# Kernel optimization log

Measured on AMD Instinct MI355X. Metric: run time of the kernel, lower is better.

Reference implementation:

```python
import jax, jax.numpy as jnp
import numpy as np

BATCH = 2048
OUT_DIM = 50257                      # output_dim = input feature dim
LEVELS = 2
LEVEL_SIZE = int(np.ceil(OUT_DIM ** (1.0 / LEVELS)))  # 225


def setup_inputs() -> dict:
    key = jax.random.key(0)
    k_x, k_w0, k_w1 = jax.random.split(key, 3)
    # glorot-ish scale for weights so softmax logits are well behaved
    w_scale = (2.0 / (OUT_DIM + LEVEL_SIZE)) ** 0.5
    return {
        "x": jax.random.normal(k_x, (BATCH, OUT_DIM), dtype=jnp.float32),
        "W0": jax.random.normal(k_w0, (OUT_DIM, LEVEL_SIZE), dtype=jnp.float32) * w_scale,
        "W1": jax.random.normal(k_w1, (OUT_DIM, LEVEL_SIZE), dtype=jnp.float32) * w_scale,
        "b0": jnp.zeros((LEVEL_SIZE,), dtype=jnp.float32),
        "b1": jnp.zeros((LEVEL_SIZE,), dtype=jnp.float32),
    }


def reference(x, W0, W1, b0, b1):
    # per-level softmax heads: [B, L]
    h0 = jax.nn.softmax(x @ W0 + b0, axis=-1)
    h1 = jax.nn.softmax(x @ W1 + b1, axis=-1)
    # outer product per sample, flattened: [B, L*L] (replaces nested theano.scan)
    path = (h0[:, :, None] * h1[:, None, :]).reshape(x.shape[0], -1)
    # truncate to output_dim, as in original output[:, :self.output_dim]
    return path[:, :OUT_DIM]
```

## Files before the change

### kernel.cpp

```cpp
#include <hip/hip_runtime.h>
#include <stdint.h>
#include <math.h>


#define BATCH   2048
#define KDIM    50257
#define LSZ     225
#define HOFF    240
#define NPAD    480
#define BK      32
#define BM      128
#define NT      1571
#define TILE_B  30720
#define A_BYTES 16384
#define BUF_B   47104
#define LDS_TOT 94208
#define WSCALE  1024.0f

typedef __attribute__((ext_vector_type(8))) _Float16 f16x8;
typedef __attribute__((ext_vector_type(4))) float    f32x4;

__device__ __forceinline__ unsigned short f2h(float f) {
  return __builtin_bit_cast(unsigned short, (_Float16)f);
}
__device__ __forceinline__ int swzr(int r) { return ((r >> 1) & 3) << 4; }

__global__ __launch_bounds__(512) void hs_prep(const float* __restrict__ W0,
                                               const float* __restrict__ W1,
                                               unsigned char* __restrict__ wt) {
  const int kt = blockIdx.x;
  const int k0 = kt * BK;
  unsigned char* tb = wt + (size_t)kt * TILE_B;
  for (int idx = threadIdx.x; idx < NPAD * 8; idx += 512) {
    const int n = idx >> 3, c4 = idx & 7;
    const float* src = nullptr;
    if (n < HOFF) { if (n < LSZ) src = W0 + n; }
    else          { if (n - HOFF < LSZ) src = W1 + (n - HOFF); }
    unsigned short he[4];
#pragma unroll
    for (int e = 0; e < 4; ++e) {
      const int k = k0 + c4 * 4 + e;
      float v = (src != nullptr && k < KDIM) ? src[(size_t)k * LSZ] * WSCALE : 0.0f;
      he[e] = f2h(v);
    }
    const int jp = (c4 * 8) ^ swzr(n);
    *(ushort4*)(tb + n * 64 + jp) = make_ushort4(he[0], he[1], he[2], he[3]);
  }
}

__global__ __launch_bounds__(512, 2) void hs_gemm(
    const float* __restrict__ x, const unsigned char* __restrict__ wt,
    float* __restrict__ partials, int ksplit, int tpc) {
  extern __shared__ __align__(16) unsigned char smem[];
  const int bid   = blockIdx.x;
  const int chunk = bid % ksplit;
  const int mtile = bid / ksplit;
  const int t0 = chunk * tpc;
  int t1 = t0 + tpc; if (t1 > NT) t1 = NT;
  const int m0 = mtile * BM;
  const int tid = threadIdx.x;
  const int lane = tid & 63, wid = tid >> 6;
  const int wm = wid >> 1, wn = wid & 1;
  const int jl  = (lane >> 4) * 16;
  const int l15 = lane & 15;

  const int arow0 = tid >> 3, c4 = tid & 7;
  const int arow1 = arow0 + 64;
  const float* xr0 = x + (size_t)(m0 + arow0) * KDIM + c4 * 4;
  const float* xr1 = xr0 + (size_t)64 * KDIM;
  const int aoff0 = arow0 * 64 + ((c4 * 8) ^ swzr(arow0));
  const int aoff1 = arow1 * 64 + ((c4 * 8) ^ swzr(arow1));

  f32x4 acc[2][15];
#pragma unroll
  for (int mf = 0; mf < 2; ++mf)
#pragma unroll
    for (int nf = 0; nf < 15; ++nf)
      acc[mf][nf] = f32x4{0.f, 0.f, 0.f, 0.f};

  auto stageB = [&](int kt, int buf) {
    const unsigned char* src = wt + (size_t)kt * TILE_B + lane * 16;
    unsigned char* dstb = smem + buf * BUF_B;
#pragma unroll
    for (int c = 0; c < 4; ++c) {
      const int cc = wid + c * 8;
      if (cc < 30) {
        __builtin_amdgcn_global_load_lds(
            (const __attribute__((address_space(1))) unsigned int*)(src + cc * 1024),
            (__attribute__((address_space(3))) unsigned int*)(dstb + cc * 1024),
            16, 0, 0);
      }
    }
  };

  auto loadA = [&](int kt, f32x4& v0, f32x4& v1) {
    const int kb = kt * BK + c4 * 4;
    const float* p0 = xr0 + (size_t)kt * BK;
    const float* p1 = xr1 + (size_t)kt * BK;
    if (kb + 4 <= KDIM) {
      __builtin_memcpy(&v0, p0, 16);
      __builtin_memcpy(&v1, p1, 16);
    } else {
#pragma unroll
      for (int e = 0; e < 4; ++e) {
        v0[e] = (kb + e < KDIM) ? p0[e] : 0.f;
        v1[e] = (kb + e < KDIM) ? p1[e] : 0.f;
      }
    }
  };

  auto writeA = [&](int buf, const f32x4& v0, const f32x4& v1) {
    unsigned char* ab = smem + buf * BUF_B + TILE_B;
    unsigned short h0e[4], l0e[4], h1e[4], l1e[4];
#pragma unroll
    for (int e = 0; e < 4; ++e) {
      const _Float16 h = (_Float16)v0[e];
      h0e[e] = __builtin_bit_cast(unsigned short, h);
      l0e[e] = f2h(v0[e] - (float)h);
      const _Float16 g = (_Float16)v1[e];
      h1e[e] = __builtin_bit_cast(unsigned short, g);
      l1e[e] = f2h(v1[e] - (float)g);
    }
    *(ushort4*)(ab + aoff0)        = make_ushort4(h0e[0], h0e[1], h0e[2], h0e[3]);
    *(ushort4*)(ab + 8192 + aoff0) = make_ushort4(l0e[0], l0e[1], l0e[2], l0e[3]);
    *(ushort4*)(ab + aoff1)        = make_ushort4(h1e[0], h1e[1], h1e[2], h1e[3]);
    *(ushort4*)(ab + 8192 + aoff1) = make_ushort4(l1e[0], l1e[1], l1e[2], l1e[3]);
  };

  auto compute = [&](int buf) {
    const unsigned char* bb = smem + buf * BUF_B;
    const unsigned char* ab = bb + TILE_B;
    f16x8 ah[2], al[2];
#pragma unroll
    for (int mf = 0; mf < 2; ++mf) {
      const int m = wm * 32 + mf * 16 + l15;
      const int off = m * 64 + (jl ^ swzr(m));
      ah[mf] = *(const f16x8*)(ab + off);
      al[mf] = *(const f16x8*)(ab + 8192 + off);
    }
#pragma unroll
    for (int nf = 0; nf < 15; ++nf) {
      const int n = wn * 240 + nf * 16 + l15;
      const int off = n * 64 + (jl ^ swzr(n));
      const f16x8 bw = *(const f16x8*)(bb + off);
#pragma unroll
      for (int mf = 0; mf < 2; ++mf) {
        acc[mf][nf] = __builtin_amdgcn_mfma_f32_16x16x32_f16(ah[mf], bw, acc[mf][nf], 0, 0, 0);
        acc[mf][nf] = __builtin_amdgcn_mfma_f32_16x16x32_f16(al[mf], bw, acc[mf][nf], 0, 0, 0);
      }
    }
  };

  if (t0 < t1) {
    f32x4 v0, v1;
    stageB(t0, 0);
    loadA(t0, v0, v1);
    writeA(0, v0, v1);
    __syncthreads();
    int buf = 0;
    for (int t = t0; t < t1; ++t) {
      const bool more = (t + 1 < t1);
      if (more) {
        stageB(t + 1, buf ^ 1);
        loadA(t + 1, v0, v1);
      }
      compute(buf);
      if (more) writeA(buf ^ 1, v0, v1);
      __syncthreads();
      buf ^= 1;
    }
  }

  float* pout = partials + ((size_t)chunk * BATCH + m0) * NPAD;
#pragma unroll
  for (int mf = 0; mf < 2; ++mf)
#pragma unroll
    for (int nf = 0; nf < 15; ++nf)
#pragma unroll
      for (int r = 0; r < 4; ++r) {
        const int row = wm * 32 + mf * 16 + (lane >> 4) * 4 + r;
        const int col = wn * 240 + nf * 16 + l15;
        pout[(size_t)row * NPAD + col] = acc[mf][nf][r];
      }
}

__global__ __launch_bounds__(512) void hs_finish(
    const float* __restrict__ partials, const float* __restrict__ b0,
    const float* __restrict__ b1, float* __restrict__ out, int ksplit) {
  const int b = blockIdx.x;
  __shared__ float lg[NPAD];
  __shared__ float red[4];
  const int tid = threadIdx.x;
  if (tid < NPAD) {
    float v = 0.f;
    for (int c = 0; c < ksplit; ++c)
      v += partials[((size_t)c * BATCH + b) * NPAD + tid];
    v *= (1.0f / WSCALE);
    if (tid < LSZ) v += b0[tid];
    else if (tid >= HOFF && tid < HOFF + LSZ) v += b1[tid - HOFF];
    lg[tid] = v;
  }
  __syncthreads();
  const int wid = tid >> 6, lane = tid & 63;
  if (wid < 2) {
    const int base = wid * HOFF;
    float m = -1e30f;
    for (int i = lane; i < LSZ; i += 64) m = fmaxf(m, lg[base + i]);
#pragma unroll
    for (int s = 32; s; s >>= 1) m = fmaxf(m, __shfl_xor(m, s));
    float sum = 0.f;
    for (int i = lane; i < LSZ; i += 64) sum += __expf(lg[base + i] - m);
#pragma unroll
    for (int s = 32; s; s >>= 1) sum += __shfl_xor(sum, s);
    if (lane == 0) { red[wid * 2] = m; red[wid * 2 + 1] = 1.0f / sum; }
  }
  __syncthreads();
  if (tid < NPAD) {
    const int h = (tid >= HOFF) ? 1 : 0;
    const int off = tid - (h ? HOFF : 0);
    float hv = 0.f;
    if (off < LSZ) hv = __expf(lg[tid] - red[2 * h]) * red[2 * h + 1];
    lg[tid] = hv;
  }
  __syncthreads();
  const size_t ob = (size_t)b * KDIM;
  for (int f = tid; f < KDIM; f += 512) {
    const int i = f / LSZ;
    const int j = f - i * LSZ;
    out[ob + f] = lg[i] * lg[HOFF + j];
  }
}

extern "C" void kernel_launch(void* const* d_in, const int* in_sizes, int n_in,
                              void* d_out, int out_size, void* d_ws, size_t ws_size,
                              hipStream_t stream) {
  (void)in_sizes; (void)n_in; (void)out_size;
  const float* x  = (const float*)d_in[0];
  const float* W0 = (const float*)d_in[1];
  const float* W1 = (const float*)d_in[2];
  const float* b0 = (const float*)d_in[3];
  const float* b1 = (const float*)d_in[4];
  float* out = (float*)d_out;
  unsigned char* ws = (unsigned char*)d_ws;

  const size_t WT_BYTES  = (size_t)NT * TILE_B;
  const size_t PER_CHUNK = (size_t)BATCH * NPAD * sizeof(float);
  int ksplit = 16;
  if (ws_size > WT_BYTES) {
    const int kmax = (int)((ws_size - WT_BYTES) / PER_CHUNK);
    if (ksplit > kmax) ksplit = kmax;
  } else {
    ksplit = 1;
  }
  if (ksplit < 1) ksplit = 1;
  float* partials = (float*)(ws + WT_BYTES);
  const int tpc = (NT + ksplit - 1) / ksplit;

  hs_prep<<<dim3(NT), dim3(512), 0, stream>>>(W0, W1, ws);
  hipFuncSetAttribute((const void*)hs_gemm,
                      hipFuncAttributeMaxDynamicSharedMemorySize, LDS_TOT);
  hs_gemm<<<dim3(16 * ksplit), dim3(512), LDS_TOT, stream>>>(x, ws, partials, ksplit, tpc);
  hs_finish<<<dim3(BATCH), dim3(512), 0, stream>>>(partials, b0, b1, out, ksplit);
}
```

Before: 349.9 us.

## Load A fragments directly from global into MFMA registers, skip LDS staging

```diff
diff --git a/kernel.cpp b/kernel.cpp
--- a/kernel.cpp
+++ b/kernel.cpp
@@ -12,9 +12,8 @@
 #define BM      128
 #define NT      1571
 #define TILE_B  30720
-#define A_BYTES 16384
-#define BUF_B   47104
-#define LDS_TOT 94208
+#define BUF_B   30720
+#define LDS_TOT 61440
 #define WSCALE  1024.0f
 
 typedef __attribute__((ext_vector_type(8))) _Float16 f16x8;
@@ -24,6 +23,8 @@
   return __builtin_bit_cast(unsigned short, (_Float16)f);
 }
 __device__ __forceinline__ int swzr(int r) { return ((r >> 1) & 3) << 4; }
+
+#define ASM_VMCNT0() asm volatile("s_waitcnt vmcnt(0)" ::: "memory")
 
 __global__ __launch_bounds__(512) void hs_prep(const float* __restrict__ W0,
                                                const float* __restrict__ W1,
@@ -62,14 +63,11 @@
   const int lane = tid & 63, wid = tid >> 6;
   const int wm = wid >> 1, wn = wid & 1;
   const int jl  = (lane >> 4) * 16;
+  const int ko  = (lane >> 4) * 8;
   const int l15 = lane & 15;
 
-  const int arow0 = tid >> 3, c4 = tid & 7;
-  const int arow1 = arow0 + 64;
-  const float* xr0 = x + (size_t)(m0 + arow0) * KDIM + c4 * 4;
-  const float* xr1 = xr0 + (size_t)64 * KDIM;
-  const int aoff0 = arow0 * 64 + ((c4 * 8) ^ swzr(arow0));
-  const int aoff1 = arow1 * 64 + ((c4 * 8) ^ swzr(arow1));
+  const float* ar0 = x + (size_t)(m0 + wm * 32 + l15) * KDIM + ko;
+  const float* ar1 = ar0 + (size_t)16 * KDIM;
 
   f32x4 acc[2][15];
 #pragma unroll
@@ -77,6 +75,9 @@
 #pragma unroll
     for (int nf = 0; nf < 15; ++nf)
       acc[mf][nf] = f32x4{0.f, 0.f, 0.f, 0.f};
+
+  f32x4 g00, g01, g10, g11;
+  f16x8 ah0, al0, ah1, al1;
 
   auto stageB = [&](int kt, int buf) {
     const unsigned char* src = wt + (size_t)kt * TILE_B + lane * 16;
@@ -93,79 +94,70 @@
     }
   };
 
-  auto loadA = [&](int kt, f32x4& v0, f32x4& v1) {
-    const int kb = kt * BK + c4 * 4;
-    const float* p0 = xr0 + (size_t)kt * BK;
-    const float* p1 = xr1 + (size_t)kt * BK;
-    if (kb + 4 <= KDIM) {
-      __builtin_memcpy(&v0, p0, 16);
-      __builtin_memcpy(&v1, p1, 16);
+  auto gloadA = [&](int kt) {
+    const int kb = kt * BK + ko;
+    const float* p0 = ar0 + (size_t)kt * BK;
+    const float* p1 = ar1 + (size_t)kt * BK;
+    if (kb + 8 <= KDIM) {
+      __builtin_memcpy(&g00, p0, 16);  __builtin_memcpy(&g01, p0 + 4, 16);
+      __builtin_memcpy(&g10, p1, 16);  __builtin_memcpy(&g11, p1 + 4, 16);
     } else {
 #pragma unroll
       for (int e = 0; e < 4; ++e) {
-        v0[e] = (kb + e < KDIM) ? p0[e] : 0.f;
-        v1[e] = (kb + e < KDIM) ? p1[e] : 0.f;
-      }
-    }
-  };
-
-  auto writeA = [&](int buf, const f32x4& v0, const f32x4& v1) {
-    unsigned char* ab = smem + buf * BUF_B + TILE_B;
-    unsigned short h0e[4], l0e[4], h1e[4], l1e[4];
+        g00[e] = (kb + e < KDIM)     ? p0[e]     : 0.f;
+        g01[e] = (kb + 4 + e < KDIM) ? p0[4 + e] : 0.f;
+        g10[e] = (kb + e < KDIM)     ? p1[e]     : 0.f;
+        g11[e] = (kb + 4 + e < KDIM) ? p1[4 + e] : 0.f;
+      }
+    }
+  };
+
+  auto convertA = [&]() {
 #pragma unroll
     for (int e = 0; e < 4; ++e) {
-      const _Float16 h = (_Float16)v0[e];
-      h0e[e] = __builtin_bit_cast(unsigned short, h);
-      l0e[e] = f2h(v0[e] - (float)h);
-      const _Float16 g = (_Float16)v1[e];
-      h1e[e] = __builtin_bit_cast(unsigned short, g);
-      l1e[e] = f2h(v1[e] - (float)g);
-    }
-    *(ushort4*)(ab + aoff0)        = make_ushort4(h0e[0], h0e[1], h0e[2], h0e[3]);
-    *(ushort4*)(ab + 8192 + aoff0) = make_ushort4(l0e[0], l0e[1], l0e[2], l0e[3]);
-    *(ushort4*)(ab + aoff1)        = make_ushort4(h1e[0], h1e[1], h1e[2], h1e[3]);
-    *(ushort4*)(ab + 8192 + aoff1) = make_ushort4(l1e[0], l1e[1], l1e[2], l1e[3]);
+      const _Float16 h0 = (_Float16)g00[e];
+      ah0[e] = h0;          al0[e] = (_Float16)(g00[e] - (float)h0);
+      const _Float16 h1 = (_Float16)g01[e];
+      ah0[4 + e] = h1;      al0[4 + e] = (_Float16)(g01[e] - (float)h1);
+      const _Float16 h2 = (_Float16)g10[e];
+      ah1[e] = h2;          al1[e] = (_Float16)(g10[e] - (float)h2);
+      const _Float16 h3 = (_Float16)g11[e];
+      ah1[4 + e] = h3;      al1[4 + e] = (_Float16)(g11[e] - (float)h3);
+    }
   };
 
   auto compute = [&](int buf) {
     const unsigned char* bb = smem + buf * BUF_B;
-    const unsigned char* ab = bb + TILE_B;
-    f16x8 ah[2], al[2];
-#pragma unroll
-    for (int mf = 0; mf < 2; ++mf) {
-      const int m = wm * 32 + mf * 16 + l15;
-      const int off = m * 64 + (jl ^ swzr(m));
-      ah[mf] = *(const f16x8*)(ab + off);
-      al[mf] = *(const f16x8*)(ab + 8192 + off);
-    }
 #pragma unroll
     for (int nf = 0; nf < 15; ++nf) {
       const int n = wn * 240 + nf * 16 + l15;
       const int off = n * 64 + (jl ^ swzr(n));
       const f16x8 bw = *(const f16x8*)(bb + off);
-#pragma unroll
-      for (int mf = 0; mf < 2; ++mf) {
-        acc[mf][nf] = __builtin_amdgcn_mfma_f32_16x16x32_f16(ah[mf], bw, acc[mf][nf], 0, 0, 0);
-        acc[mf][nf] = __builtin_amdgcn_mfma_f32_16x16x32_f16(al[mf], bw, acc[mf][nf], 0, 0, 0);
-      }
+      acc[0][nf] = __builtin_amdgcn_mfma_f32_16x16x32_f16(ah0, bw, acc[0][nf], 0, 0, 0);
+      acc[0][nf] = __builtin_amdgcn_mfma_f32_16x16x32_f16(al0, bw, acc[0][nf], 0, 0, 0);
+      acc[1][nf] = __builtin_amdgcn_mfma_f32_16x16x32_f16(ah1, bw, acc[1][nf], 0, 0, 0);
+      acc[1][nf] = __builtin_amdgcn_mfma_f32_16x16x32_f16(al1, bw, acc[1][nf], 0, 0, 0);
     }
   };
 
   if (t0 < t1) {
-    f32x4 v0, v1;
     stageB(t0, 0);
-    loadA(t0, v0, v1);
-    writeA(0, v0, v1);
+    gloadA(t0);
+    ASM_VMCNT0();
+    convertA();
     __syncthreads();
     int buf = 0;
     for (int t = t0; t < t1; ++t) {
       const bool more = (t + 1 < t1);
       if (more) {
         stageB(t + 1, buf ^ 1);
-        loadA(t + 1, v0, v1);
+        gloadA(t + 1);
       }
       compute(buf);
-      if (more) writeA(buf ^ 1, v0, v1);
+      if (more) {
+        ASM_VMCNT0();
+        convertA();
+      }
       __syncthreads();
       buf ^= 1;
     }
```

New measurement: 373.8 us. 1.07x slower.

## Use 12 waves per GEMM block with a 4x3 warp grid to cut accumulators

Applied to the files above, without the earlier changes.

```diff
diff --git a/kernel.cpp b/kernel.cpp
--- a/kernel.cpp
+++ b/kernel.cpp
@@ -48,7 +48,7 @@
   }
 }
 
-__global__ __launch_bounds__(512, 2) void hs_gemm(
+__global__ __launch_bounds__(768, 3) void hs_gemm(
     const float* __restrict__ x, const unsigned char* __restrict__ wt,
     float* __restrict__ partials, int ksplit, int tpc) {
   extern __shared__ __align__(16) unsigned char smem[];
@@ -60,30 +60,28 @@
   const int m0 = mtile * BM;
   const int tid = threadIdx.x;
   const int lane = tid & 63, wid = tid >> 6;
-  const int wm = wid >> 1, wn = wid & 1;
+  const int wm = wid & 3, wn = wid >> 2;
   const int jl  = (lane >> 4) * 16;
   const int l15 = lane & 15;
 
-  const int arow0 = tid >> 3, c4 = tid & 7;
-  const int arow1 = arow0 + 64;
-  const float* xr0 = x + (size_t)(m0 + arow0) * KDIM + c4 * 4;
-  const float* xr1 = xr0 + (size_t)64 * KDIM;
-  const int aoff0 = arow0 * 64 + ((c4 * 8) ^ swzr(arow0));
-  const int aoff1 = arow1 * 64 + ((c4 * 8) ^ swzr(arow1));
-
-  f32x4 acc[2][15];
+  const int arow = tid >> 2, c8 = tid & 3;
+  const bool astg = (tid < 512);
+  const float* xr = x + (size_t)(m0 + arow) * KDIM + c8 * 8;
+  const int aoff = arow * 64 + ((c8 * 16) ^ swzr(arow));
+
+  f32x4 acc[2][10];
 #pragma unroll
   for (int mf = 0; mf < 2; ++mf)
 #pragma unroll
-    for (int nf = 0; nf < 15; ++nf)
+    for (int nf = 0; nf < 10; ++nf)
       acc[mf][nf] = f32x4{0.f, 0.f, 0.f, 0.f};
 
   auto stageB = [&](int kt, int buf) {
     const unsigned char* src = wt + (size_t)kt * TILE_B + lane * 16;
     unsigned char* dstb = smem + buf * BUF_B;
 #pragma unroll
-    for (int c = 0; c < 4; ++c) {
-      const int cc = wid + c * 8;
+    for (int c = 0; c < 3; ++c) {
+      const int cc = wid + c * 12;
       if (cc < 30) {
         __builtin_amdgcn_global_load_lds(
             (const __attribute__((address_space(1))) unsigned int*)(src + cc * 1024),
@@ -94,37 +92,38 @@
   };
 
   auto loadA = [&](int kt, f32x4& v0, f32x4& v1) {
-    const int kb = kt * BK + c4 * 4;
-    const float* p0 = xr0 + (size_t)kt * BK;
-    const float* p1 = xr1 + (size_t)kt * BK;
-    if (kb + 4 <= KDIM) {
-      __builtin_memcpy(&v0, p0, 16);
-      __builtin_memcpy(&v1, p1, 16);
+    if (!astg) return;
+    const int kb = kt * BK + c8 * 8;
+    const float* p = xr + (size_t)kt * BK;
+    if (kb + 8 <= KDIM) {
+      __builtin_memcpy(&v0, p, 16);
+      __builtin_memcpy(&v1, p + 4, 16);
     } else {
 #pragma unroll
       for (int e = 0; e < 4; ++e) {
-        v0[e] = (kb + e < KDIM) ? p0[e] : 0.f;
-        v1[e] = (kb + e < KDIM) ? p1[e] : 0.f;
+        v0[e] = (kb + e < KDIM)     ? p[e]     : 0.f;
+        v1[e] = (kb + 4 + e < KDIM) ? p[4 + e] : 0.f;
       }
     }
   };
 
   auto writeA = [&](int buf, const f32x4& v0, const f32x4& v1) {
+    if (!astg) return;
     unsigned char* ab = smem + buf * BUF_B + TILE_B;
-    unsigned short h0e[4], l0e[4], h1e[4], l1e[4];
+    unsigned short he[8], le[8];
 #pragma unroll
     for (int e = 0; e < 4; ++e) {
       const _Float16 h = (_Float16)v0[e];
-      h0e[e] = __builtin_bit_cast(unsigned short, h);
-      l0e[e] = f2h(v0[e] - (float)h);
+      he[e] = __builtin_bit_cast(unsigned short, h);
+      le[e] = f2h(v0[e] - (float)h);
       const _Float16 g = (_Float16)v1[e];
-      h1e[e] = __builtin_bit_cast(unsigned short, g);
-      l1e[e] = f2h(v1[e] - (float)g);
-    }
-    *(ushort4*)(ab + aoff0)        = make_ushort4(h0e[0], h0e[1], h0e[2], h0e[3]);
-    *(ushort4*)(ab + 8192 + aoff0) = make_ushort4(l0e[0], l0e[1], l0e[2], l0e[3]);
-    *(ushort4*)(ab + aoff1)        = make_ushort4(h1e[0], h1e[1], h1e[2], h1e[3]);
-    *(ushort4*)(ab + 8192 + aoff1) = make_ushort4(l1e[0], l1e[1], l1e[2], l1e[3]);
+      he[4 + e] = __builtin_bit_cast(unsigned short, g);
+      le[4 + e] = f2h(v1[e] - (float)g);
+    }
+    *(ushort4*)(ab + aoff)            = make_ushort4(he[0], he[1], he[2], he[3]);
+    *(ushort4*)(ab + aoff + 8)        = make_ushort4(he[4], he[5], he[6], he[7]);
+    *(ushort4*)(ab + 8192 + aoff)     = make_ushort4(le[0], le[1], le[2], le[3]);
+    *(ushort4*)(ab + 8192 + aoff + 8) = make_ushort4(le[4], le[5], le[6], le[7]);
   };
 
   auto compute = [&](int buf) {
@@ -139,8 +138,8 @@
       al[mf] = *(const f16x8*)(ab + 8192 + off);
     }
 #pragma unroll
-    for (int nf = 0; nf < 15; ++nf) {
-      const int n = wn * 240 + nf * 16 + l15;
+    for (int nf = 0; nf < 10; ++nf) {
+      const int n = wn * 160 + nf * 16 + l15;
       const int off = n * 64 + (jl ^ swzr(n));
       const f16x8 bw = *(const f16x8*)(bb + off);
 #pragma unroll
@@ -175,11 +174,11 @@
 #pragma unroll
   for (int mf = 0; mf < 2; ++mf)
 #pragma unroll
-    for (int nf = 0; nf < 15; ++nf)
+    for (int nf = 0; nf < 10; ++nf)
 #pragma unroll
       for (int r = 0; r < 4; ++r) {
         const int row = wm * 32 + mf * 16 + (lane >> 4) * 4 + r;
-        const int col = wn * 240 + nf * 16 + l15;
+        const int col = wn * 160 + nf * 16 + l15;
         pout[(size_t)row * NPAD + col] = acc[mf][nf][r];
       }
 }
@@ -259,6 +258,6 @@
   hs_prep<<<dim3(NT), dim3(512), 0, stream>>>(W0, W1, ws);
   hipFuncSetAttribute((const void*)hs_gemm,
                       hipFuncAttributeMaxDynamicSharedMemorySize, LDS_TOT);
-  hs_gemm<<<dim3(16 * ksplit), dim3(512), LDS_TOT, stream>>>(x, ws, partials, ksplit, tpc);
+  hs_gemm<<<dim3(16 * ksplit), dim3(768), LDS_TOT, stream>>>(x, ws, partials, ksplit, tpc);
   hs_finish<<<dim3(BATCH), dim3(512), 0, stream>>>(partials, b0, b1, out, ksplit);
 }
```

Result: no change. 346.3 us (-1.0%).

## Drop x hi/lo fp16 split and double the K tile to 64

Applied to the files above, without the earlier changes.

```diff
diff --git a/kernel.cpp b/kernel.cpp
--- a/kernel.cpp
+++ b/kernel.cpp
@@ -8,13 +8,13 @@
 #define LSZ     225
 #define HOFF    240
 #define NPAD    480
-#define BK      32
+#define BK      64
 #define BM      128
-#define NT      1571
-#define TILE_B  30720
+#define NT      786
+#define TILE_B  61440
 #define A_BYTES 16384
-#define BUF_B   47104
-#define LDS_TOT 94208
+#define BUF_B   77824
+#define LDS_TOT 155648
 #define WSCALE  1024.0f
 
 typedef __attribute__((ext_vector_type(8))) _Float16 f16x8;
@@ -23,7 +23,7 @@
 __device__ __forceinline__ unsigned short f2h(float f) {
   return __builtin_bit_cast(unsigned short, (_Float16)f);
 }
-__device__ __forceinline__ int swzr(int r) { return ((r >> 1) & 3) << 4; }
+__device__ __forceinline__ int swz8(int r) { return (r & 7) << 4; }
 
 __global__ __launch_bounds__(512) void hs_prep(const float* __restrict__ W0,
                                                const float* __restrict__ W1,
@@ -31,8 +31,8 @@
   const int kt = blockIdx.x;
   const int k0 = kt * BK;
   unsigned char* tb = wt + (size_t)kt * TILE_B;
-  for (int idx = threadIdx.x; idx < NPAD * 8; idx += 512) {
-    const int n = idx >> 3, c4 = idx & 7;
+  for (int idx = threadIdx.x; idx < NPAD * 16; idx += 512) {
+    const int n = idx >> 4, c4 = idx & 15;
     const float* src = nullptr;
     if (n < HOFF) { if (n < LSZ) src = W0 + n; }
     else          { if (n - HOFF < LSZ) src = W1 + (n - HOFF); }
@@ -43,8 +43,8 @@
       float v = (src != nullptr && k < KDIM) ? src[(size_t)k * LSZ] * WSCALE : 0.0f;
       he[e] = f2h(v);
     }
-    const int jp = (c4 * 8) ^ swzr(n);
-    *(ushort4*)(tb + n * 64 + jp) = make_ushort4(he[0], he[1], he[2], he[3]);
+    const int jp = (c4 * 8) ^ swz8(n);
+    *(ushort4*)(tb + n * 128 + jp) = make_ushort4(he[0], he[1], he[2], he[3]);
   }
 }
 
@@ -64,12 +64,8 @@
   const int jl  = (lane >> 4) * 16;
   const int l15 = lane & 15;
 
-  const int arow0 = tid >> 3, c4 = tid & 7;
-  const int arow1 = arow0 + 64;
-  const float* xr0 = x + (size_t)(m0 + arow0) * KDIM + c4 * 4;
-  const float* xr1 = xr0 + (size_t)64 * KDIM;
-  const int aoff0 = arow0 * 64 + ((c4 * 8) ^ swzr(arow0));
-  const int aoff1 = arow1 * 64 + ((c4 * 8) ^ swzr(arow1));
+  const int arow = tid >> 2, c16 = tid & 3;
+  const float* xr = x + (size_t)(m0 + arow) * KDIM + c16 * 16;
 
   f32x4 acc[2][15];
 #pragma unroll
@@ -82,9 +78,9 @@
     const unsigned char* src = wt + (size_t)kt * TILE_B + lane * 16;
     unsigned char* dstb = smem + buf * BUF_B;
 #pragma unroll
-    for (int c = 0; c < 4; ++c) {
+    for (int c = 0; c < 8; ++c) {
       const int cc = wid + c * 8;
-      if (cc < 30) {
+      if (cc < 60) {
         __builtin_amdgcn_global_load_lds(
             (const __attribute__((address_space(1))) unsigned int*)(src + cc * 1024),
             (__attribute__((address_space(3))) unsigned int*)(dstb + cc * 1024),
@@ -93,79 +89,76 @@
     }
   };
 
-  auto loadA = [&](int kt, f32x4& v0, f32x4& v1) {
-    const int kb = kt * BK + c4 * 4;
-    const float* p0 = xr0 + (size_t)kt * BK;
-    const float* p1 = xr1 + (size_t)kt * BK;
-    if (kb + 4 <= KDIM) {
-      __builtin_memcpy(&v0, p0, 16);
-      __builtin_memcpy(&v1, p1, 16);
+  auto loadA = [&](int kt, f32x4& v0, f32x4& v1, f32x4& v2, f32x4& v3) {
+    const int kb = kt * BK + c16 * 16;
+    const float* p = xr + (size_t)kt * BK;
+    if (kb + 16 <= KDIM) {
+      __builtin_memcpy(&v0, p, 16);      __builtin_memcpy(&v1, p + 4, 16);
+      __builtin_memcpy(&v2, p + 8, 16);  __builtin_memcpy(&v3, p + 12, 16);
     } else {
 #pragma unroll
       for (int e = 0; e < 4; ++e) {
-        v0[e] = (kb + e < KDIM) ? p0[e] : 0.f;
-        v1[e] = (kb + e < KDIM) ? p1[e] : 0.f;
-      }
-    }
-  };
-
-  auto writeA = [&](int buf, const f32x4& v0, const f32x4& v1) {
-    unsigned char* ab = smem + buf * BUF_B + TILE_B;
-    unsigned short h0e[4], l0e[4], h1e[4], l1e[4];
+        v0[e] = (kb + e < KDIM)      ? p[e]      : 0.f;
+        v1[e] = (kb + 4 + e < KDIM)  ? p[4 + e]  : 0.f;
+        v2[e] = (kb + 8 + e < KDIM)  ? p[8 + e]  : 0.f;
+        v3[e] = (kb + 12 + e < KDIM) ? p[12 + e] : 0.f;
+      }
+    }
+  };
+
+  auto writeA = [&](int buf, const f32x4& v0, const f32x4& v1,
+                    const f32x4& v2, const f32x4& v3) {
+    unsigned char* ab = smem + buf * BUF_B + TILE_B + arow * 128;
+    unsigned short he[16];
 #pragma unroll
     for (int e = 0; e < 4; ++e) {
-      const _Float16 h = (_Float16)v0[e];
-      h0e[e] = __builtin_bit_cast(unsigned short, h);
-      l0e[e] = f2h(v0[e] - (float)h);
-      const _Float16 g = (_Float16)v1[e];
-      h1e[e] = __builtin_bit_cast(unsigned short, g);
-      l1e[e] = f2h(v1[e] - (float)g);
-    }
-    *(ushort4*)(ab + aoff0)        = make_ushort4(h0e[0], h0e[1], h0e[2], h0e[3]);
-    *(ushort4*)(ab + 8192 + aoff0) = make_ushort4(l0e[0], l0e[1], l0e[2], l0e[3]);
-    *(ushort4*)(ab + aoff1)        = make_ushort4(h1e[0], h1e[1], h1e[2], h1e[3]);
-    *(ushort4*)(ab + 8192 + aoff1) = make_ushort4(l1e[0], l1e[1], l1e[2], l1e[3]);
+      he[e]      = f2h(v0[e]);
+      he[4 + e]  = f2h(v1[e]);
+      he[8 + e]  = f2h(v2[e]);
+      he[12 + e] = f2h(v3[e]);
+    }
+    const int s = swz8(arow);
+    __builtin_memcpy(ab + ((c16 * 32) ^ s),      he,     16);
+    __builtin_memcpy(ab + ((c16 * 32 + 16) ^ s), he + 8, 16);
   };
 
   auto compute = [&](int buf) {
     const unsigned char* bb = smem + buf * BUF_B;
     const unsigned char* ab = bb + TILE_B;
-    f16x8 ah[2], al[2];
-#pragma unroll
-    for (int mf = 0; mf < 2; ++mf) {
-      const int m = wm * 32 + mf * 16 + l15;
-      const int off = m * 64 + (jl ^ swzr(m));
-      ah[mf] = *(const f16x8*)(ab + off);
-      al[mf] = *(const f16x8*)(ab + 8192 + off);
-    }
-#pragma unroll
-    for (int nf = 0; nf < 15; ++nf) {
-      const int n = wn * 240 + nf * 16 + l15;
-      const int off = n * 64 + (jl ^ swzr(n));
-      const f16x8 bw = *(const f16x8*)(bb + off);
+#pragma unroll
+    for (int ks = 0; ks < 2; ++ks) {
+      const int kbyte = ks * 64 + jl;
+      f16x8 ah[2];
 #pragma unroll
       for (int mf = 0; mf < 2; ++mf) {
-        acc[mf][nf] = __builtin_amdgcn_mfma_f32_16x16x32_f16(ah[mf], bw, acc[mf][nf], 0, 0, 0);
-        acc[mf][nf] = __builtin_amdgcn_mfma_f32_16x16x32_f16(al[mf], bw, acc[mf][nf], 0, 0, 0);
+        const int m = wm * 32 + mf * 16 + l15;
+        ah[mf] = *(const f16x8*)(ab + m * 128 + (kbyte ^ swz8(m)));
+      }
+#pragma unroll
+      for (int nf = 0; nf < 15; ++nf) {
+        const int n = wn * 240 + nf * 16 + l15;
+        const f16x8 bw = *(const f16x8*)(bb + n * 128 + (kbyte ^ swz8(n)));
+        acc[0][nf] = __builtin_amdgcn_mfma_f32_16x16x32_f16(ah[0], bw, acc[0][nf], 0, 0, 0);
+        acc[1][nf] = __builtin_amdgcn_mfma_f32_16x16x32_f16(ah[1], bw, acc[1][nf], 0, 0, 0);
       }
     }
   };
 
   if (t0 < t1) {
-    f32x4 v0, v1;
+    f32x4 v0, v1, v2, v3;
     stageB(t0, 0);
-    loadA(t0, v0, v1);
-    writeA(0, v0, v1);
+    loadA(t0, v0, v1, v2, v3);
+    writeA(0, v0, v1, v2, v3);
     __syncthreads();
     int buf = 0;
     for (int t = t0; t < t1; ++t) {
       const bool more = (t + 1 < t1);
       if (more) {
         stageB(t + 1, buf ^ 1);
-        loadA(t + 1, v0, v1);
+        loadA(t + 1, v0, v1, v2, v3);
       }
       compute(buf);
-      if (more) writeA(buf ^ 1, v0, v1);
+      if (more) writeA(buf ^ 1, v0, v1, v2, v3);
       __syncthreads();
       buf ^= 1;
     }
```

Result: faster. 323.7 us, median of 2 (-7.5%).
